# Optimization experiments

Measured on AMD Instinct MI355X. Metric: run time of the kernel, lower is better.

## Reference

```python
import jax, jax.numpy as jnp
import numpy as np

POOL = 7
NUM_ROIS = 256
SCALE = 1.0 / 16.0  # feature-map stride
H, W, C = 128, 128, 1024
STRIDE = 16


def setup_inputs() -> dict:
    key = jax.random.key(0)
    k_img, k_wh, k_xy = jax.random.split(key, 3)
    img = jax.random.normal(k_img, (1, H, W, C), dtype=jnp.float32)
    # ROIs in image-pixel units (x, y, w, h); w,h >= 16 so crop >= 1 feature cell
    max_px = H * STRIDE  # 2048
    wh = jax.random.uniform(k_wh, (1, NUM_ROIS, 2), minval=16.0, maxval=max_px * 0.5)
    xy = jax.random.uniform(k_xy, (1, NUM_ROIS, 2), minval=0.0, maxval=1.0) * (max_px - wh)
    rois = jnp.concatenate([xy, wh], axis=-1).astype(jnp.float32)
    return {"img": img, "rois": rois}


def _pool_one_roi(img0, roi):
    # img0: (H, W, C); roi: (4,) = (x, y, w, h) in pixels.
    # Original: int cast of scaled coords, crop img[y:y+h, x:x+w],
    # then TF1 bilinear resize (align_corners=False, src = i * in/out).
    c = (roi * SCALE).astype(jnp.int32)  # truncation == floor for positive coords
    x0, y0, w, h = c[0], c[1], c[2], c[3]
    i = jnp.arange(POOL, dtype=jnp.float32)
    # source coords within the cropped section
    sy = i * (h.astype(jnp.float32) / POOL)
    sx = i * (w.astype(jnp.float32) / POOL)
    fy = jnp.floor(sy)
    fx = jnp.floor(sx)
    ty = sy - fy  # (P,) lerp weights
    tx = sx - fx
    y_lo = fy.astype(jnp.int32)
    x_lo = fx.astype(jnp.int32)
    y_hi = jnp.minimum(y_lo + 1, jnp.maximum(h - 1, 0))  # clamp at section edge
    x_hi = jnp.minimum(x_lo + 1, jnp.maximum(w - 1, 0))
    gy0 = jnp.clip(y0 + y_lo, 0, H - 1)
    gy1 = jnp.clip(y0 + y_hi, 0, H - 1)
    gx0 = jnp.clip(x0 + x_lo, 0, W - 1)
    gx1 = jnp.clip(x0 + x_hi, 0, W - 1)
    v00 = img0[gy0[:, None], gx0[None, :]]  # (P, P, C)
    v01 = img0[gy0[:, None], gx1[None, :]]
    v10 = img0[gy1[:, None], gx0[None, :]]
    v11 = img0[gy1[:, None], gx1[None, :]]
    top = v00 + tx[None, :, None] * (v01 - v00)
    bot = v10 + tx[None, :, None] * (v11 - v10)
    return top + ty[:, None, None] * (bot - top)  # (P, P, C)


def reference(img, rois):
    img0 = img[0]  # (H, W, C)
    pooled = jax.vmap(lambda r: _pool_one_roi(img0, r))(rois[0])  # (NR, P, P, C)
    return pooled[None]  # (1, num_rois, pool, pool, C)
```

## Files before the change

kernel.cpp:

```cpp
#include <hip/hip_runtime.h>


#define IMG_H 128
#define IMG_W 128
#define IMG_C 1024
#define POOLK 7

typedef float vfloat4 __attribute__((ext_vector_type(4)));

__device__ __forceinline__ vfloat4 lerp2d(vfloat4 v00, vfloat4 v01,
                                          vfloat4 v10, vfloat4 v11,
                                          float tx, float ty) {
  vfloat4 top = v00 + tx * (v01 - v00);
  vfloat4 bot = v10 + tx * (v11 - v10);
  return top + ty * (bot - top);
}

__global__ __launch_bounds__(128) void roi_pool_kernel(
    const float* __restrict__ img,
    const float* __restrict__ rois,
    float* __restrict__ out) {
  const int ix = blockIdx.x;
  const int iy = blockIdx.y;
  const int r  = blockIdx.z;

  const vfloat4 roi = *(const vfloat4*)(rois + (size_t)r * 4);

  const int x0 = (int)(roi.x * 0.0625f);
  const int y0 = (int)(roi.y * 0.0625f);
  const int w  = (int)(roi.z * 0.0625f);
  const int h  = (int)(roi.w * 0.0625f);

  const float sy = (float)iy * ((float)h / 7.0f);
  const float sx = (float)ix * ((float)w / 7.0f);
  const float fy = floorf(sy);
  const float fx = floorf(sx);
  const float ty = sy - fy;
  const float tx = sx - fx;
  const int y_lo = (int)fy;
  const int x_lo = (int)fx;
  const int y_hi = min(y_lo + 1, max(h - 1, 0));
  const int x_hi = min(x_lo + 1, max(w - 1, 0));
  const int gy0 = min(max(y0 + y_lo, 0), IMG_H - 1);
  const int gy1 = min(max(y0 + y_hi, 0), IMG_H - 1);
  const int gx0 = min(max(x0 + x_lo, 0), IMG_W - 1);
  const int gx1 = min(max(x0 + x_hi, 0), IMG_W - 1);

  const int c = threadIdx.x * 8;

  const float* p00 = img + ((size_t)(gy0 * IMG_W + gx0)) * IMG_C + c;
  const float* p01 = img + ((size_t)(gy0 * IMG_W + gx1)) * IMG_C + c;
  const float* p10 = img + ((size_t)(gy1 * IMG_W + gx0)) * IMG_C + c;
  const float* p11 = img + ((size_t)(gy1 * IMG_W + gx1)) * IMG_C + c;

  const vfloat4 a00 = *(const vfloat4*)(p00);
  const vfloat4 b00 = *(const vfloat4*)(p00 + 4);
  const vfloat4 a01 = *(const vfloat4*)(p01);
  const vfloat4 b01 = *(const vfloat4*)(p01 + 4);
  const vfloat4 a10 = *(const vfloat4*)(p10);
  const vfloat4 b10 = *(const vfloat4*)(p10 + 4);
  const vfloat4 a11 = *(const vfloat4*)(p11);
  const vfloat4 b11 = *(const vfloat4*)(p11 + 4);

  const vfloat4 oa = lerp2d(a00, a01, a10, a11, tx, ty);
  const vfloat4 ob = lerp2d(b00, b01, b10, b11, tx, ty);

  float* op = out + (((size_t)r * POOLK + iy) * POOLK + ix) * IMG_C + c;
  *(vfloat4*)op = oa;
  *(vfloat4*)(op + 4) = ob;
}

extern "C" void kernel_launch(void* const* d_in, const int* in_sizes, int n_in,
                              void* d_out, int out_size, void* d_ws, size_t ws_size,
                              hipStream_t stream) {
  const float* img  = (const float*)d_in[0];
  const float* rois = (const float*)d_in[1];
  float* out = (float*)d_out;

  dim3 grid(POOLK, POOLK, 256);
  dim3 block(128);
  roi_pool_kernel<<<grid, block, 0, stream>>>(img, rois, out);
}
```

Measured before the change: 120.1 us.

## Process a full output row per block, looping over pooled x positions

Each block now handles one pooled row (iy) of one ROI and loops over the seven x positions, with 256 threads each covering four channels instead of 128 threads covering eight. The y-side coordinate math and row pointers are computed once per block instead of once per output cell. This cuts the grid from 12544 blocks to 1792, lowering launch and per-block setup cost and letting loads of shared columns within a row be reused from cache. The tradeoff is fewer blocks, which may reduce parallelism and the number of memory requests in flight for this bandwidth-bound gather.

```diff
diff --git a/kernel.cpp b/kernel.cpp
--- a/kernel.cpp
+++ b/kernel.cpp
@@ -5,24 +5,16 @@
 #define IMG_W 128
 #define IMG_C 1024
 #define POOLK 7
+#define NROIS 256
 
 typedef float vfloat4 __attribute__((ext_vector_type(4)));
 
-__device__ __forceinline__ vfloat4 lerp2d(vfloat4 v00, vfloat4 v01,
-                                          vfloat4 v10, vfloat4 v11,
-                                          float tx, float ty) {
-  vfloat4 top = v00 + tx * (v01 - v00);
-  vfloat4 bot = v10 + tx * (v11 - v10);
-  return top + ty * (bot - top);
-}
-
-__global__ __launch_bounds__(128) void roi_pool_kernel(
+__global__ __launch_bounds__(256) void roi_pool_kernel(
     const float* __restrict__ img,
     const float* __restrict__ rois,
     float* __restrict__ out) {
-  const int ix = blockIdx.x;
-  const int iy = blockIdx.y;
-  const int r  = blockIdx.z;
+  const int iy = blockIdx.x;
+  const int r  = blockIdx.y;
 
   const vfloat4 roi = *(const vfloat4*)(rois + (size_t)r * 4);
 
@@ -32,42 +24,42 @@
   const int h  = (int)(roi.w * 0.0625f);
 
   const float sy = (float)iy * ((float)h / 7.0f);
-  const float sx = (float)ix * ((float)w / 7.0f);
   const float fy = floorf(sy);
-  const float fx = floorf(sx);
   const float ty = sy - fy;
-  const float tx = sx - fx;
   const int y_lo = (int)fy;
-  const int x_lo = (int)fx;
   const int y_hi = min(y_lo + 1, max(h - 1, 0));
-  const int x_hi = min(x_lo + 1, max(w - 1, 0));
   const int gy0 = min(max(y0 + y_lo, 0), IMG_H - 1);
   const int gy1 = min(max(y0 + y_hi, 0), IMG_H - 1);
-  const int gx0 = min(max(x0 + x_lo, 0), IMG_W - 1);
-  const int gx1 = min(max(x0 + x_hi, 0), IMG_W - 1);
 
-  const int c = threadIdx.x * 8;
+  const int c = threadIdx.x * 4;
+  const float* row0 = img + (size_t)gy0 * (IMG_W * IMG_C) + c;
+  const float* row1 = img + (size_t)gy1 * (IMG_W * IMG_C) + c;
+  float* orow = out + (((size_t)r * POOLK + iy) * POOLK) * IMG_C + c;
 
-  const float* p00 = img + ((size_t)(gy0 * IMG_W + gx0)) * IMG_C + c;
-  const float* p01 = img + ((size_t)(gy0 * IMG_W + gx1)) * IMG_C + c;
-  const float* p10 = img + ((size_t)(gy1 * IMG_W + gx0)) * IMG_C + c;
-  const float* p11 = img + ((size_t)(gy1 * IMG_W + gx1)) * IMG_C + c;
+  const float step_x = (float)w / 7.0f;
+  const int xmax = max(w - 1, 0);
 
-  const vfloat4 a00 = *(const vfloat4*)(p00);
-  const vfloat4 b00 = *(const vfloat4*)(p00 + 4);
-  const vfloat4 a01 = *(const vfloat4*)(p01);
-  const vfloat4 b01 = *(const vfloat4*)(p01 + 4);
-  const vfloat4 a10 = *(const vfloat4*)(p10);
-  const vfloat4 b10 = *(const vfloat4*)(p10 + 4);
-  const vfloat4 a11 = *(const vfloat4*)(p11);
-  const vfloat4 b11 = *(const vfloat4*)(p11 + 4);
+#pragma unroll
+  for (int ix = 0; ix < POOLK; ++ix) {
+    const float sx = (float)ix * step_x;
+    const float fx = floorf(sx);
+    const float tx = sx - fx;
+    const int x_lo = (int)fx;
+    const int x_hi = min(x_lo + 1, xmax);
+    const int gx0 = min(max(x0 + x_lo, 0), IMG_W - 1);
+    const int gx1 = min(max(x0 + x_hi, 0), IMG_W - 1);
 
-  const vfloat4 oa = lerp2d(a00, a01, a10, a11, tx, ty);
-  const vfloat4 ob = lerp2d(b00, b01, b10, b11, tx, ty);
+    const vfloat4 v00 = *(const vfloat4*)(row0 + (size_t)gx0 * IMG_C);
+    const vfloat4 v01 = *(const vfloat4*)(row0 + (size_t)gx1 * IMG_C);
+    const vfloat4 v10 = *(const vfloat4*)(row1 + (size_t)gx0 * IMG_C);
+    const vfloat4 v11 = *(const vfloat4*)(row1 + (size_t)gx1 * IMG_C);
 
-  float* op = out + (((size_t)r * POOLK + iy) * POOLK + ix) * IMG_C + c;
-  *(vfloat4*)op = oa;
-  *(vfloat4*)(op + 4) = ob;
+    const vfloat4 top = v00 + tx * (v01 - v00);
+    const vfloat4 bot = v10 + tx * (v11 - v10);
+    const vfloat4 o   = top + ty * (bot - top);
+
+    *(vfloat4*)(orow + (size_t)ix * IMG_C) = o;
+  }
 }
 
 extern "C" void kernel_launch(void* const* d_in, const int* in_sizes, int n_in,
@@ -77,7 +69,7 @@
   const float* rois = (const float*)d_in[1];
   float* out = (float*)d_out;
 
-  dim3 grid(POOLK, POOLK, 256);
-  dim3 block(128);
+  dim3 grid(POOLK, NROIS);
+  dim3 block(256);
   roi_pool_kernel<<<grid, block, 0, stream>>>(img, rois, out);
 }
```

New measurement: 119.6 us. About the same (-0.4%).
